# Performance work log

Hardware: AMD Instinct MI355X
Metric: run time of the kernel (lower is better)

## Reference

```python
import jax, jax.numpy as jnp
import numpy as np

N_NODES = 200000
N_EVENTS = 100000
MEM_DIM = 100
TIME_DIM = 100
MSG_DIM = 172
T_MAX = 1000000


def setup_inputs() -> dict:
    key = jax.random.key(0)
    ks = jax.random.split(key, 12)
    s = 0.05
    return {
        "memory": jax.random.normal(ks[0], (N_NODES, MEM_DIM), jnp.float32),
        "raw_msg": jax.random.normal(ks[1], (N_EVENTS, MSG_DIM), jnp.float32),
        "time_w": jax.random.normal(ks[2], (TIME_DIM, 1), jnp.float32) * s,
        "time_b": jax.random.normal(ks[3], (TIME_DIM,), jnp.float32) * s,
        "w_ih": jax.random.normal(ks[4], (3 * MEM_DIM, 2 * MEM_DIM + MSG_DIM + TIME_DIM), jnp.float32) * s,
        "w_hh": jax.random.normal(ks[5], (3 * MEM_DIM, MEM_DIM), jnp.float32) * s,
        "b_ih": jax.random.normal(ks[6], (3 * MEM_DIM,), jnp.float32) * s,
        "b_hh": jax.random.normal(ks[7], (3 * MEM_DIM,), jnp.float32) * s,
        "last_update": jax.random.randint(ks[8], (N_NODES,), 0, T_MAX, jnp.int32),
        "src": jax.random.randint(ks[9], (N_EVENTS,), 0, N_NODES, jnp.int32),
        "dst": jax.random.randint(ks[10], (N_EVENTS,), 0, N_NODES, jnp.int32),
        "t": jax.random.randint(ks[11], (N_EVENTS,), 0, T_MAX, jnp.int32),
    }


def _time_enc(t_rel, time_w, time_b):
    # Linear(1, time_dim) followed by cos, as in TGN.update_memory
    return jnp.cos(t_rel[:, None] * time_w[:, 0][None, :] + time_b[None, :])


def _gru_cell(x, h, w_ih, w_hh, b_ih, b_hh):
    gi = x @ w_ih.T + b_ih  # [N, 3*D]
    gh = h @ w_hh.T + b_hh
    i_r, i_z, i_n = jnp.split(gi, 3, axis=-1)
    h_r, h_z, h_n = jnp.split(gh, 3, axis=-1)
    r = jax.nn.sigmoid(i_r + h_r)
    z = jax.nn.sigmoid(i_z + h_z)
    n = jnp.tanh(i_n + r * h_n)
    return (1.0 - z) * n + z * h


def reference(memory, raw_msg, time_w, time_b, w_ih, w_hh, b_ih, b_hh,
              last_update, src, dst, t):
    # time-relative encodings for source- and destination-side messages
    t_rel_s = (t - last_update[src]).astype(memory.dtype)
    t_rel_d = (t - last_update[dst]).astype(memory.dtype)
    t_enc_s = _time_enc(t_rel_s, time_w, time_b)  # [E, time_dim]
    t_enc_d = _time_enc(t_rel_d, time_w, time_b)

    mem_s = memory[src]  # [E, D]
    mem_d = memory[dst]

    # IdentityMessage: concat(mem_self, mem_other, raw_msg, t_enc)
    msg_s = jnp.concatenate([mem_s, mem_d, raw_msg, t_enc_s], axis=-1)  # [E, 472]
    msg_d = jnp.concatenate([mem_d, mem_s, raw_msg, t_enc_d], axis=-1)

    idx = jnp.concatenate([src, dst], axis=0)          # [2E]
    msgs = jnp.concatenate([msg_s, msg_d], axis=0)      # [2E, 472]

    n_nodes = memory.shape[0]
    # MeanAggregator: per-node mean of incoming messages
    summed = jax.ops.segment_sum(msgs, idx, num_segments=n_nodes)  # [N, 472]
    counts = jax.ops.segment_sum(jnp.ones((idx.shape[0],), memory.dtype), idx,
                                 num_segments=n_nodes)             # [N]
    aggr = summed / jnp.maximum(counts, 1.0)[:, None]

    # GRU memory update, applied only to nodes that received messages
    h_new = _gru_cell(aggr, memory, w_ih, w_hh, b_ih, b_hh)
    touched = (counts > 0)[:, None]
    return jnp.where(touched, h_new, memory)  # [N, memory_dim]
```

## Files before the change

kernel.cpp:

```cpp
#include <hip/hip_runtime.h>
#include <math.h>

#define NND 200000
#define NEV 100000
#define MD 100
#define TD 100
#define MSGD 172
#define NB 64
#define NFRAG 25
#define KS 15
#define BP_ELEMS (KS * NFRAG * 64 * 8)
#define GLS 74

typedef __attribute__((ext_vector_type(8))) short bf16x8;
typedef __attribute__((ext_vector_type(4))) float f32x4;

__device__ __forceinline__ float fast_sigmoid(float x) {
    return 1.0f / (1.0f + __expf(-x));
}
__device__ __forceinline__ float fast_tanh(float x) {
    return fmaf(2.0f, 1.0f / (1.0f + __expf(-2.0f * x)), -1.0f);
}

__device__ __forceinline__ unsigned short f2bf(float f) {
    union { float f; unsigned int u; } v; v.f = f;
    unsigned int r = (v.u + 0x7FFFu + ((v.u >> 16) & 1u)) >> 16;
    return (unsigned short)r;
}
__device__ __forceinline__ float bf2f(unsigned int h) {
    union { unsigned int u; float f; } v; v.u = h << 16;
    return v.f;
}
__device__ __forceinline__ unsigned int pk(float a, float b) {
    unsigned int r;
    asm("v_cvt_pk_bf16_f32 %0, %1, %2" : "=v"(r) : "v"(a), "v"(b));
    return r;
}

__global__ __launch_bounds__(256) void k_count(
    const int* __restrict__ src, const int* __restrict__ dst, int* __restrict__ cnt)
{
    int e = blockIdx.x * 256 + threadIdx.x;
    if (e >= NEV) return;
    atomicAdd(&cnt[src[e]], 1);
    atomicAdd(&cnt[dst[e]], 1);
}

__global__ __launch_bounds__(256) void k_scan1(
    const int* __restrict__ cnt, int* __restrict__ off, int* __restrict__ psum)
{
    __shared__ int sdat[256];
    int t = threadIdx.x, b = blockIdx.x;
    int i0 = b * 1024 + t * 4;
    int v0 = (i0 + 0 < NND) ? cnt[i0 + 0] : 0;
    int v1 = (i0 + 1 < NND) ? cnt[i0 + 1] : 0;
    int v2 = (i0 + 2 < NND) ? cnt[i0 + 2] : 0;
    int v3 = (i0 + 3 < NND) ? cnt[i0 + 3] : 0;
    int tsum = v0 + v1 + v2 + v3;
    sdat[t] = tsum;
    __syncthreads();
    for (int o = 1; o < 256; o <<= 1) {
        int x = (t >= o) ? sdat[t - o] : 0;
        __syncthreads();
        sdat[t] += x;
        __syncthreads();
    }
    int excl = sdat[t] - tsum;
    if (i0 + 0 < NND) off[i0 + 0] = excl;
    if (i0 + 1 < NND) off[i0 + 1] = excl + v0;
    if (i0 + 2 < NND) off[i0 + 2] = excl + v0 + v1;
    if (i0 + 3 < NND) off[i0 + 3] = excl + v0 + v1 + v2;
    if (t == 255) psum[b] = sdat[255];
}

__global__ __launch_bounds__(256) void k_scan2(int* __restrict__ psum, int nblk)
{
    __shared__ int sdat[256];
    int t = threadIdx.x;
    int v = (t < nblk) ? psum[t] : 0;
    sdat[t] = v;
    __syncthreads();
    for (int o = 1; o < 256; o <<= 1) {
        int x = (t >= o) ? sdat[t - o] : 0;
        __syncthreads();
        sdat[t] += x;
        __syncthreads();
    }
    if (t < nblk) psum[t] = sdat[t] - v;
}

__global__ __launch_bounds__(256) void k_scan3(
    int* __restrict__ off, const int* __restrict__ psum, int* __restrict__ cur)
{
    int t = threadIdx.x, b = blockIdx.x;
    int base = psum[b];
    int i0 = b * 1024 + t * 4;
#pragma unroll
    for (int j = 0; j < 4; ++j) {
        int i = i0 + j;
        if (i < NND) {
            int v = off[i] + base;
            off[i] = v;
            cur[i] = v;
        }
    }
}

__global__ __launch_bounds__(256) void k_place(
    const int* __restrict__ src, const int* __restrict__ dst,
    const int* __restrict__ tarr, const int* __restrict__ last_update,
    int* __restrict__ cur, int4* __restrict__ entries)
{
    int e = blockIdx.x * 256 + threadIdx.x;
    if (e >= NEV) return;
    int s = src[e], d = dst[e], tt = tarr[e];
    int slot = atomicAdd(&cur[s], 1);
    entries[slot] = make_int4(d, e, __float_as_int((float)(tt - last_update[s])), s);
    slot = atomicAdd(&cur[d], 1);
    entries[slot] = make_int4(s, e, __float_as_int((float)(tt - last_update[d])), d);
}

__global__ __launch_bounds__(256) void tgn_prep(
    const float* __restrict__ w_ih, const float* __restrict__ w_hh,
    unsigned short* __restrict__ Bp)
{
    int idx = blockIdx.x * 256 + threadIdx.x;
    if (idx >= BP_ELEMS) return;
    int e = idx & 7;
    int lane = (idx >> 3) & 63;
    int t = idx >> 9;
    int nf = t % 25;
    int ks = t / 25;
    int col = nf * 16 + (lane & 15);
    int k = ks * 32 + ((lane >> 4) << 3) + e;
    float v = 0.0f;
    if (col < 200) {
        if (k < 472) v = w_ih[col * 472 + k];
        if (k < 100) v += w_hh[col * 100 + k];
    } else if (col < 300) {
        if (k < 472) v = w_ih[col * 472 + k];
    } else {
        if (k < 100) v = w_hh[(col - 100) * 100 + k];
    }
    Bp[idx] = f2bf(v);
}

__global__ __launch_bounds__(256) void k_memcvt(
    const float* __restrict__ memory, uint4* __restrict__ membf)
{
    int idx = blockIdx.x * 256 + threadIdx.x;
    if (idx >= NND * 13) return;
    int node = idx / 13, u = idx - node * 13;
    const float4* ms = reinterpret_cast<const float4*>(memory + (size_t)node * MD);
    uint4 o = (uint4){0u, 0u, 0u, 0u};
    if (u < 12) {
        float4 x = ms[2 * u], y = ms[2 * u + 1];
        o.x = pk(x.x, x.y); o.y = pk(x.z, x.w);
        o.z = pk(y.x, y.y); o.w = pk(y.z, y.w);
    } else {
        float4 x = ms[24];
        o.x = pk(x.x, x.y); o.y = pk(x.z, x.w);
    }
    membf[idx] = o;
}

__global__ __launch_bounds__(256) void k_rawcvt(
    const float* __restrict__ raw_msg, uint4* __restrict__ rawbf)
{
    int idx = blockIdx.x * 256 + threadIdx.x;
    if (idx >= NEV * 22) return;
    int e = idx / 22, r = idx - e * 22;
    const float4* rs = reinterpret_cast<const float4*>(raw_msg + (size_t)e * MSGD);
    float4 x = rs[2 * r];
    float4 y = (float4){0.f, 0.f, 0.f, 0.f};
    if (2 * r + 1 < 43) y = rs[2 * r + 1];
    uint4 o;
    o.x = pk(x.x, x.y); o.y = pk(x.z, x.w);
    o.z = pk(y.x, y.y); o.w = pk(y.z, y.w);
    rawbf[idx] = o;
}

__global__ __launch_bounds__(512, 4) void tgn_gemm(
    const float* __restrict__ memory, const uint4* __restrict__ membf,
    const uint4* __restrict__ rawbf, const int4* __restrict__ entries,
    const float* __restrict__ time_w, const float* __restrict__ time_b,
    const unsigned short* __restrict__ Bp,
    const float* __restrict__ b_ih, const float* __restrict__ b_hh,
    const int* __restrict__ cnt, const int* __restrict__ off,
    float* __restrict__ out)
{
    __shared__ __align__(16) unsigned short lds[64 * 480];
    __shared__ int cnt_s[NB], off_s[NB];
    int tid = threadIdx.x;
    int n0 = blockIdx.x * NB;

    if (tid < NB) {
        cnt_s[tid] = cnt[n0 + tid];
        off_s[tid] = off[n0 + tid];
    }
    __syncthreads();

    int lane = tid & 63;
    int wv = tid >> 6;

    {
        int u = lane;
        bool lOther = (u >= 13 && u <= 24);
        bool lRaw   = (u >= 25 && u <= 45);
        bool lMix   = (u == 12);
        bool lR46   = (u == 46);
        bool lTenc  = (u >= 47 && u <= 58);
        int offA = lOther ? (16 * u - 200) : (16 * u - 400);

        float tw[8], tb[8];
#pragma unroll
        for (int j = 0; j < 8; ++j) { tw[j] = 0.f; tb[j] = 0.f; }
        if (lTenc) {
            int d0 = 8 * u - 372;
            float4 wa = *reinterpret_cast<const float4*>(time_w + d0);
            float4 wb = *reinterpret_cast<const float4*>(time_w + d0 + 4);
            float4 ba = *reinterpret_cast<const float4*>(time_b + d0);
            float4 bb = *reinterpret_cast<const float4*>(time_b + d0 + 4);
            tw[0] = wa.x; tw[1] = wa.y; tw[2] = wa.z; tw[3] = wa.w;
            tw[4] = wb.x; tw[5] = wb.y; tw[6] = wb.z; tw[7] = wb.w;
            tb[0] = ba.x; tb[1] = ba.y; tb[2] = ba.z; tb[3] = ba.w;
            tb[4] = bb.x; tb[5] = bb.y; tb[6] = bb.z; tb[7] = bb.w;
        } else if (lR46) {
            float4 wa = *reinterpret_cast<const float4*>(time_w);
            float4 ba = *reinterpret_cast<const float4*>(time_b);
            tw[4] = wa.x; tw[5] = wa.y; tw[6] = wa.z; tw[7] = wa.w;
            tb[4] = ba.x; tb[5] = ba.y; tb[6] = ba.z; tb[7] = ba.w;
        }

        const char* membc = reinterpret_cast<const char*>(membf);
        const char* rawbc = reinterpret_cast<const char*>(rawbf);

#pragma unroll
        for (int half = 0; half < 2; ++half) {
            int rb = wv * 8 + half * 4;
            int cc[4], oo[4];
#pragma unroll
            for (int r = 0; r < 4; ++r) { cc[r] = cnt_s[rb + r]; oo[r] = off_s[rb + r]; }
            int4 en[4];
#pragma unroll
            for (int r = 0; r < 4; ++r)
                en[r] = (cc[r] > 0) ? entries[oo[r]] : make_int4(0, 0, 0, 0);
            uint4 mreg[4];
#pragma unroll
            for (int r = 0; r < 4; ++r)
                mreg[r] = (u < 13) ? membf[(size_t)(n0 + rb + r) * 13 + u]
                                   : (uint4){0u, 0u, 0u, 0u};
            uint2 gA[4], gB[4];
#pragma unroll
            for (int r = 0; r < 4; ++r) {
                gA[r] = (uint2){0u, 0u}; gB[r] = (uint2){0u, 0u};
                if (cc[r] > 0) {
                    if (lOther) {
                        const char* p = membc + (size_t)en[r].x * 208 + offA;
                        gA[r] = *reinterpret_cast<const uint2*>(p);
                        gB[r] = *reinterpret_cast<const uint2*>(p + 8);
                    } else if (lMix) {
                        gB[r] = *reinterpret_cast<const uint2*>(membc + (size_t)en[r].x * 208);
                    } else if (lRaw) {
                        const char* p = rawbc + (size_t)en[r].y * 352 + offA;
                        gA[r] = *reinterpret_cast<const uint2*>(p);
                        gB[r] = *reinterpret_cast<const uint2*>(p + 8);
                    } else if (lR46) {
                        gA[r] = *reinterpret_cast<const uint2*>(rawbc + (size_t)en[r].y * 352 + 336);
                    }
                }
            }
#pragma unroll
            for (int r = 0; r < 4; ++r) {
                int c = cc[r];
                float a0 = bf2f(gA[r].x & 0xffffu), a1 = bf2f(gA[r].x >> 16);
                float a2 = bf2f(gA[r].y & 0xffffu), a3 = bf2f(gA[r].y >> 16);
                float a4 = bf2f(gB[r].x & 0xffffu), a5 = bf2f(gB[r].x >> 16);
                float a6 = bf2f(gB[r].y & 0xffffu), a7 = bf2f(gB[r].y >> 16);
                if ((lTenc || lR46) && c > 0) {
                    float trel = __int_as_float(en[r].z);
                    if (lTenc) {
                        a0 = __cosf(fmaf(trel, tw[0], tb[0]));
                        a1 = __cosf(fmaf(trel, tw[1], tb[1]));
                        a2 = __cosf(fmaf(trel, tw[2], tb[2]));
                        a3 = __cosf(fmaf(trel, tw[3], tb[3]));
                    }
                    a4 = __cosf(fmaf(trel, tw[4], tb[4]));
                    a5 = __cosf(fmaf(trel, tw[5], tb[5]));
                    a6 = __cosf(fmaf(trel, tw[6], tb[6]));
                    a7 = __cosf(fmaf(trel, tw[7], tb[7]));
                }
                for (int i = 1; i < c; ++i) {
                    int4 e2 = entries[oo[r] + i];
                    uint2 hA = (uint2){0u, 0u}, hB = (uint2){0u, 0u};
                    if (lOther) {
                        const char* p = membc + (size_t)e2.x * 208 + offA;
                        hA = *reinterpret_cast<const uint2*>(p);
                        hB = *reinterpret_cast<const uint2*>(p + 8);
                    } else if (lMix) {
                        hB = *reinterpret_cast<const uint2*>(membc + (size_t)e2.x * 208);
                    } else if (lRaw) {
                        const char* p = rawbc + (size_t)e2.y * 352 + offA;
                        hA = *reinterpret_cast<const uint2*>(p);
                        hB = *reinterpret_cast<const uint2*>(p + 8);
                    } else if (lR46) {
                        hA = *reinterpret_cast<const uint2*>(rawbc + (size_t)e2.y * 352 + 336);
                    }
                    a0 += bf2f(hA.x & 0xffffu); a1 += bf2f(hA.x >> 16);
                    a2 += bf2f(hA.y & 0xffffu); a3 += bf2f(hA.y >> 16);
                    a4 += bf2f(hB.x & 0xffffu); a5 += bf2f(hB.x >> 16);
                    a6 += bf2f(hB.y & 0xffffu); a7 += bf2f(hB.y >> 16);
                    if (lTenc || lR46) {
                        float trel = __int_as_float(e2.z);
                        if (lTenc) {
                            a0 += __cosf(fmaf(trel, tw[0], tb[0]));
                            a1 += __cosf(fmaf(trel, tw[1], tb[1]));
                            a2 += __cosf(fmaf(trel, tw[2], tb[2]));
                            a3 += __cosf(fmaf(trel, tw[3], tb[3]));
                        }
                        a4 += __cosf(fmaf(trel, tw[4], tb[4]));
                        a5 += __cosf(fmaf(trel, tw[5], tb[5]));
                        a6 += __cosf(fmaf(trel, tw[6], tb[6]));
                        a7 += __cosf(fmaf(trel, tw[7], tb[7]));
                    }
                }
                float ci = 1.0f / fmaxf((float)c, 1.0f);
                uint4 o;
                if (u < 12) {
                    o = mreg[r];
                } else if (u == 12) {
                    o.x = mreg[r].x; o.y = mreg[r].y;
                    o.z = pk(a4 * ci, a5 * ci); o.w = pk(a6 * ci, a7 * ci);
                } else {
                    o.x = pk(a0 * ci, a1 * ci); o.y = pk(a2 * ci, a3 * ci);
                    o.z = pk(a4 * ci, a5 * ci); o.w = pk(a6 * ci, a7 * ci);
                }
                if (u < 60) {
                    int nl = rb + r;
                    int byte = (nl * 960 + 16 * u) ^ ((nl & 7) << 4);
                    *reinterpret_cast<uint4*>(reinterpret_cast<char*>(lds) + byte) = o;
                }
            }
        }
    }
    __syncthreads();

    int l15 = lane & 15;
    int kg8 = (lane >> 4) << 3;
    int f0 = (wv == 0) ? 0 : (4 + 3 * (wv - 1));
    int cw = (wv == 0) ? 4 : 3;

    f32x4 acc[4][4];
#pragma unroll
    for (int g = 0; g < 4; ++g)
#pragma unroll
        for (int i = 0; i < 4; ++i) acc[g][i] = (f32x4){0.f, 0.f, 0.f, 0.f};

    const bf16x8* BpB = reinterpret_cast<const bf16x8*>(Bp);
    const char* ldsc = reinterpret_cast<const char*>(lds);

#pragma unroll
    for (int ks = 0; ks < KS; ++ks) {
        int k0 = ks * 32 + kg8;
        const bf16x8* bp = BpB + ((size_t)(ks * NFRAG + f0)) * 64 + lane;
        bf16x8 b[4];
#pragma unroll
        for (int i = 0; i < 4; ++i)
            if (i < cw) b[i] = bp[i * 64];
#pragma unroll
        for (int g = 0; g < 4; ++g) {
            int r = g * 16 + l15;
            int ab = (r * 960 + 2 * k0) ^ ((r & 7) << 4);
            bf16x8 a = *reinterpret_cast<const bf16x8*>(ldsc + ab);
#pragma unroll
            for (int i = 0; i < 4; ++i)
                if (i < cw)
                    acc[g][i] = __builtin_amdgcn_mfma_f32_16x16x32_bf16(a, b[i], acc[g][i], 0, 0, 0);
        }
    }

    float mv[13];
#pragma unroll
    for (int t = 0; t < 13; ++t) {
        int idx = tid + t * 512;
        mv[t] = (idx < NB * MD) ? memory[(size_t)n0 * MD + idx] : 0.f;
    }

    __syncthreads();

    unsigned short* Gl = lds;
    int kq = (lane >> 4) << 2;
#pragma unroll
    for (int i = 0; i < 4; ++i) {
        if (i < cw) {
            int col = (f0 + i) * 16 + l15;
            float bias = (col < 200) ? (b_ih[col] + b_hh[col])
                       : (col < 300) ? b_ih[col] : b_hh[col - 100];
#pragma unroll
            for (int g = 0; g < 4; ++g) {
                int node = g * 16 + kq;
#pragma unroll
                for (int rp = 0; rp < 2; ++rp) {
                    *reinterpret_cast<unsigned int*>(&Gl[col * GLS + node + 2 * rp]) =
                        pk(acc[g][i][2 * rp] + bias, acc[g][i][2 * rp + 1] + bias);
                }
            }
        }
    }
    __syncthreads();

#pragma unroll
    for (int t = 0; t < 13; ++t) {
        int idx = tid + t * 512;
        if (idx < NB * MD) {
            int n = idx / MD, j = idx - n * MD;
            float rp = bf2f((unsigned int)Gl[j * GLS + n]);
            float zp = bf2f((unsigned int)Gl[(100 + j) * GLS + n]);
            float inp = bf2f((unsigned int)Gl[(200 + j) * GLS + n]);
            float hnp = bf2f((unsigned int)Gl[(300 + j) * GLS + n]);
            float r = fast_sigmoid(rp);
            float z = fast_sigmoid(zp);
            float nn = fast_tanh(fmaf(r, hnp, inp));
            float h = (1.0f - z) * nn + z * mv[t];
            out[(size_t)n0 * MD + idx] = (cnt_s[n] > 0) ? h : mv[t];
        }
    }
}

extern "C" void kernel_launch(void* const* d_in, const int* in_sizes, int n_in,
                              void* d_out, int out_size, void* d_ws, size_t ws_size,
                              hipStream_t stream)
{
    const float* memory      = (const float*)d_in[0];
    const float* raw_msg     = (const float*)d_in[1];
    const float* time_w      = (const float*)d_in[2];
    const float* time_b      = (const float*)d_in[3];
    const float* w_ih        = (const float*)d_in[4];
    const float* w_hh        = (const float*)d_in[5];
    const float* b_ih        = (const float*)d_in[6];
    const float* b_hh        = (const float*)d_in[7];
    const int*   last_update = (const int*)d_in[8];
    const int*   src         = (const int*)d_in[9];
    const int*   dst         = (const int*)d_in[10];
    const int*   tarr        = (const int*)d_in[11];
    float* out = (float*)d_out;

    int* cnt  = (int*)d_ws;
    int* off  = cnt + NND;
    int* cur  = off + NND;
    int* psum = cur + NND;
    int4* entries = (int4*)(psum + 256);
    uint4* membf = (uint4*)(entries + 2 * NEV);
    uint4* rawbf = membf + (size_t)NND * 13;
    unsigned short* Bp = (unsigned short*)(rawbf + (size_t)NEV * 22);
    size_t need = (size_t)((char*)(Bp + BP_ELEMS) - (char*)d_ws);
    if (ws_size < need) return;

    const int NBLK = (NND + 1023) / 1024;
    const int NTILE = NND / NB;

    hipMemsetAsync(cnt, 0, NND * sizeof(int), stream);
    tgn_prep<<<(BP_ELEMS + 255) / 256, 256, 0, stream>>>(w_ih, w_hh, Bp);
    k_memcvt<<<(NND * 13 + 255) / 256, 256, 0, stream>>>(memory, membf);
    k_rawcvt<<<(NEV * 22 + 255) / 256, 256, 0, stream>>>(raw_msg, rawbf);
    k_count<<<(NEV + 255) / 256, 256, 0, stream>>>(src, dst, cnt);
    k_scan1<<<NBLK, 256, 0, stream>>>(cnt, off, psum);
    k_scan2<<<1, 256, 0, stream>>>(psum, NBLK);
    k_scan3<<<NBLK, 256, 0, stream>>>(off, psum, cur);
    k_place<<<(NEV + 255) / 256, 256, 0, stream>>>(src, dst, tarr, last_update, cur, entries);
    tgn_gemm<<<NTILE, 512, 0, stream>>>(memory, membf, rawbf, entries, time_w, time_b,
                                        Bp, b_ih, b_hh, cnt, off, out);
}
```

Baseline: 290.3 us.

## Fuse conversion kernels, stage entries in LDS, read epilogue memory as bf16

Merges the weight, memory and raw-message bf16 conversion kernels into one launch to cut launch overhead. The GEMM kernel stages each tile's contiguous entry range in shared memory and prefetches the next entry in the per-node aggregation loop to hide gather latency. The GRU epilogue reads node memory from the bf16 copy instead of fp32, halving that traffic but adding bf16 rounding error to the h term.

After: 262.4 us. 1.11x faster.

```diff
diff --git a/kernel.cpp b/kernel.cpp
--- a/kernel.cpp
+++ b/kernel.cpp
@@ -11,6 +11,7 @@
 #define KS 15
 #define BP_ELEMS (KS * NFRAG * 64 * 8)
 #define GLS 74
+#define ENT_CAP 256
 
 typedef __attribute__((ext_vector_type(8))) short bf16x8;
 typedef __attribute__((ext_vector_type(4))) float f32x4;
@@ -120,68 +121,65 @@
     entries[slot] = make_int4(s, e, __float_as_int((float)(tt - last_update[d])), d);
 }
 
-__global__ __launch_bounds__(256) void tgn_prep(
+__global__ __launch_bounds__(256) void k_convert(
     const float* __restrict__ w_ih, const float* __restrict__ w_hh,
-    unsigned short* __restrict__ Bp)
+    const float* __restrict__ memory, const float* __restrict__ raw_msg,
+    unsigned short* __restrict__ Bp, uint4* __restrict__ membf,
+    uint4* __restrict__ rawbf)
 {
     int idx = blockIdx.x * 256 + threadIdx.x;
-    if (idx >= BP_ELEMS) return;
-    int e = idx & 7;
-    int lane = (idx >> 3) & 63;
-    int t = idx >> 9;
-    int nf = t % 25;
-    int ks = t / 25;
-    int col = nf * 16 + (lane & 15);
-    int k = ks * 32 + ((lane >> 4) << 3) + e;
-    float v = 0.0f;
-    if (col < 200) {
-        if (k < 472) v = w_ih[col * 472 + k];
-        if (k < 100) v += w_hh[col * 100 + k];
-    } else if (col < 300) {
-        if (k < 472) v = w_ih[col * 472 + k];
-    } else {
-        if (k < 100) v = w_hh[(col - 100) * 100 + k];
-    }
-    Bp[idx] = f2bf(v);
-}
-
-__global__ __launch_bounds__(256) void k_memcvt(
-    const float* __restrict__ memory, uint4* __restrict__ membf)
-{
-    int idx = blockIdx.x * 256 + threadIdx.x;
-    if (idx >= NND * 13) return;
-    int node = idx / 13, u = idx - node * 13;
-    const float4* ms = reinterpret_cast<const float4*>(memory + (size_t)node * MD);
-    uint4 o = (uint4){0u, 0u, 0u, 0u};
-    if (u < 12) {
-        float4 x = ms[2 * u], y = ms[2 * u + 1];
+    if (idx < BP_ELEMS) {
+        int e = idx & 7;
+        int lane = (idx >> 3) & 63;
+        int t = idx >> 9;
+        int nf = t % 25;
+        int ks = t / 25;
+        int col = nf * 16 + (lane & 15);
+        int k = ks * 32 + ((lane >> 4) << 3) + e;
+        float v = 0.0f;
+        if (col < 200) {
+            if (k < 472) v = w_ih[col * 472 + k];
+            if (k < 100) v += w_hh[col * 100 + k];
+        } else if (col < 300) {
+            if (k < 472) v = w_ih[col * 472 + k];
+        } else {
+            if (k < 100) v = w_hh[(col - 100) * 100 + k];
+        }
+        Bp[idx] = f2bf(v);
+        return;
+    }
+    int j = idx - BP_ELEMS;
+    if (j < NND * 13) {
+        int node = j / 13, u = j - node * 13;
+        const float4* ms = reinterpret_cast<const float4*>(memory + (size_t)node * MD);
+        uint4 o = (uint4){0u, 0u, 0u, 0u};
+        if (u < 12) {
+            float4 x = ms[2 * u], y = ms[2 * u + 1];
+            o.x = pk(x.x, x.y); o.y = pk(x.z, x.w);
+            o.z = pk(y.x, y.y); o.w = pk(y.z, y.w);
+        } else {
+            float4 x = ms[24];
+            o.x = pk(x.x, x.y); o.y = pk(x.z, x.w);
+        }
+        membf[j] = o;
+        return;
+    }
+    j -= NND * 13;
+    if (j < NEV * 22) {
+        int e = j / 22, r = j - e * 22;
+        const float4* rs = reinterpret_cast<const float4*>(raw_msg + (size_t)e * MSGD);
+        float4 x = rs[2 * r];
+        float4 y = (float4){0.f, 0.f, 0.f, 0.f};
+        if (2 * r + 1 < 43) y = rs[2 * r + 1];
+        uint4 o;
         o.x = pk(x.x, x.y); o.y = pk(x.z, x.w);
         o.z = pk(y.x, y.y); o.w = pk(y.z, y.w);
-    } else {
-        float4 x = ms[24];
-        o.x = pk(x.x, x.y); o.y = pk(x.z, x.w);
-    }
-    membf[idx] = o;
-}
-
-__global__ __launch_bounds__(256) void k_rawcvt(
-    const float* __restrict__ raw_msg, uint4* __restrict__ rawbf)
-{
-    int idx = blockIdx.x * 256 + threadIdx.x;
-    if (idx >= NEV * 22) return;
-    int e = idx / 22, r = idx - e * 22;
-    const float4* rs = reinterpret_cast<const float4*>(raw_msg + (size_t)e * MSGD);
-    float4 x = rs[2 * r];
-    float4 y = (float4){0.f, 0.f, 0.f, 0.f};
-    if (2 * r + 1 < 43) y = rs[2 * r + 1];
-    uint4 o;
-    o.x = pk(x.x, x.y); o.y = pk(x.z, x.w);
-    o.z = pk(y.x, y.y); o.w = pk(y.z, y.w);
-    rawbf[idx] = o;
+        rawbf[j] = o;
+    }
 }
 
 __global__ __launch_bounds__(512, 4) void tgn_gemm(
-    const float* __restrict__ memory, const uint4* __restrict__ membf,
+    const uint4* __restrict__ membf,
     const uint4* __restrict__ rawbf, const int4* __restrict__ entries,
     const float* __restrict__ time_w, const float* __restrict__ time_b,
     const unsigned short* __restrict__ Bp,
@@ -191,17 +189,29 @@
 {
     __shared__ __align__(16) unsigned short lds[64 * 480];
     __shared__ int cnt_s[NB], off_s[NB];
+    __shared__ __align__(16) int4 ent_s[ENT_CAP];
     int tid = threadIdx.x;
     int n0 = blockIdx.x * NB;
 
+    int s0 = off[n0];
+    int s1 = (n0 + NB < NND) ? off[n0 + NB] : (2 * NEV);
+    int m = s1 - s0;
+    bool lds_ok = (m <= ENT_CAP);
     if (tid < NB) {
         cnt_s[tid] = cnt[n0 + tid];
         off_s[tid] = off[n0 + tid];
     }
+    if (lds_ok) {
+        for (int i = tid; i < m; i += 512) ent_s[i] = entries[s0 + i];
+    }
     __syncthreads();
 
     int lane = tid & 63;
     int wv = tid >> 6;
+
+    auto getent = [&](int slot) -> int4 {
+        return lds_ok ? ent_s[slot - s0] : entries[slot];
+    };
 
     {
         int u = lane;
@@ -244,7 +254,7 @@
             int4 en[4];
 #pragma unroll
             for (int r = 0; r < 4; ++r)
-                en[r] = (cc[r] > 0) ? entries[oo[r]] : make_int4(0, 0, 0, 0);
+                en[r] = (cc[r] > 0) ? getent(oo[r]) : make_int4(0, 0, 0, 0);
             uint4 mreg[4];
 #pragma unroll
             for (int r = 0; r < 4; ++r)
@@ -290,28 +300,30 @@
                     a6 = __cosf(fmaf(trel, tw[6], tb[6]));
                     a7 = __cosf(fmaf(trel, tw[7], tb[7]));
                 }
+                int4 e2 = (c > 1) ? getent(oo[r] + 1) : en[r];
                 for (int i = 1; i < c; ++i) {
-                    int4 e2 = entries[oo[r] + i];
+                    int4 ecur = e2;
+                    if (i + 1 < c) e2 = getent(oo[r] + i + 1);
                     uint2 hA = (uint2){0u, 0u}, hB = (uint2){0u, 0u};
                     if (lOther) {
-                        const char* p = membc + (size_t)e2.x * 208 + offA;
+                        const char* p = membc + (size_t)ecur.x * 208 + offA;
                         hA = *reinterpret_cast<const uint2*>(p);
                         hB = *reinterpret_cast<const uint2*>(p + 8);
                     } else if (lMix) {
-                        hB = *reinterpret_cast<const uint2*>(membc + (size_t)e2.x * 208);
+                        hB = *reinterpret_cast<const uint2*>(membc + (size_t)ecur.x * 208);
                     } else if (lRaw) {
-                        const char* p = rawbc + (size_t)e2.y * 352 + offA;
+                        const char* p = rawbc + (size_t)ecur.y * 352 + offA;
                         hA = *reinterpret_cast<const uint2*>(p);
                         hB = *reinterpret_cast<const uint2*>(p + 8);
                     } else if (lR46) {
-                        hA = *reinterpret_cast<const uint2*>(rawbc + (size_t)e2.y * 352 + 336);
+                        hA = *reinterpret_cast<const uint2*>(rawbc + (size_t)ecur.y * 352 + 336);
                     }
                     a0 += bf2f(hA.x & 0xffffu); a1 += bf2f(hA.x >> 16);
                     a2 += bf2f(hA.y & 0xffffu); a3 += bf2f(hA.y >> 16);
                     a4 += bf2f(hB.x & 0xffffu); a5 += bf2f(hB.x >> 16);
                     a6 += bf2f(hB.y & 0xffffu); a7 += bf2f(hB.y >> 16);
                     if (lTenc || lR46) {
-                        float trel = __int_as_float(e2.z);
+                        float trel = __int_as_float(ecur.z);
                         if (lTenc) {
                             a0 += __cosf(fmaf(trel, tw[0], tb[0]));
                             a1 += __cosf(fmaf(trel, tw[1], tb[1]));
@@ -380,10 +392,20 @@
     }
 
     float mv[13];
-#pragma unroll
-    for (int t = 0; t < 13; ++t) {
-        int idx = tid + t * 512;
-        mv[t] = (idx < NB * MD) ? memory[(size_t)n0 * MD + idx] : 0.f;
+    {
+        const char* membc = reinterpret_cast<const char*>(membf);
+#pragma unroll
+        for (int t = 0; t < 13; ++t) {
+            int idx = tid + t * 512;
+            if (idx < NB * MD) {
+                int n = idx / MD, j = idx - n * MD;
+                unsigned short h = *reinterpret_cast<const unsigned short*>(
+                    membc + (size_t)(n0 + n) * 208 + 2 * j);
+                mv[t] = bf2f((unsigned int)h);
+            } else {
+                mv[t] = 0.f;
+            }
+        }
     }
 
     __syncthreads();
@@ -458,16 +480,16 @@
 
     const int NBLK = (NND + 1023) / 1024;
     const int NTILE = NND / NB;
+    const int CVT_TOTAL = BP_ELEMS + NND * 13 + NEV * 22;
 
     hipMemsetAsync(cnt, 0, NND * sizeof(int), stream);
-    tgn_prep<<<(BP_ELEMS + 255) / 256, 256, 0, stream>>>(w_ih, w_hh, Bp);
-    k_memcvt<<<(NND * 13 + 255) / 256, 256, 0, stream>>>(memory, membf);
-    k_rawcvt<<<(NEV * 22 + 255) / 256, 256, 0, stream>>>(raw_msg, rawbf);
+    k_convert<<<(CVT_TOTAL + 255) / 256, 256, 0, stream>>>(w_ih, w_hh, memory, raw_msg,
+                                                           Bp, membf, rawbf);
     k_count<<<(NEV + 255) / 256, 256, 0, stream>>>(src, dst, cnt);
     k_scan1<<<NBLK, 256, 0, stream>>>(cnt, off, psum);
     k_scan2<<<1, 256, 0, stream>>>(psum, NBLK);
     k_scan3<<<NBLK, 256, 0, stream>>>(off, psum, cur);
     k_place<<<(NEV + 255) / 256, 256, 0, stream>>>(src, dst, tarr, last_update, cur, entries);
-    tgn_gemm<<<NTILE, 512, 0, stream>>>(memory, membf, rawbf, entries, time_w, time_b,
+    tgn_gemm<<<NTILE, 512, 0, stream>>>(membf, rawbf, entries, time_w, time_b,
                                         Bp, b_ih, b_hh, cnt, off, out);
 }
```
